# Optimization experiments

Measured on AMD Instinct MI355X. Metric: run time of the kernel, lower is better.

## Reference

```python
import jax, jax.numpy as jnp
import numpy as np

DIM = 1024
NUM_HEADS = 16
HEAD_DIM = DIM // NUM_HEADS
INNER_ITR = 4
INNER_LR = 1.0
SCALE_QKV = 1.0


def setup_inputs() -> dict:
    key = jax.random.key(0)
    k1, k2, k3 = jax.random.split(key, 3)
    B, N, C = 8, 1024, DIM
    x = jax.random.normal(k1, (B, N, C), dtype=jnp.float32)
    # Xavier-uniform-ish scaled dense kernels
    w_qkv = jax.random.normal(k2, (C, 3 * C), dtype=jnp.float32) * (1.0 / np.sqrt(C))
    w_proj = jax.random.normal(k3, (C, C), dtype=jnp.float32) * (1.0 / np.sqrt(C))
    b_proj = jnp.zeros((C,), dtype=jnp.float32)
    return {"x": x, "w_qkv": w_qkv, "w_proj": w_proj, "b_proj": b_proj, "training": 0}


def _mttt_base(q, k, v):
    """MTTT 'base' inner loop: per (B,H) linear model W,b trained by
    INNER_ITR full-batch GD steps on MSE reconstruction of v from k,
    then applied to q. Shapes: q,k,v are (B, H, N, d)."""
    B, H, N, d = q.shape
    W = jnp.zeros((B, H, d, d), dtype=q.dtype)
    b = jnp.zeros((B, H, 1, d), dtype=q.dtype)
    invN = 1.0 / N
    for _ in range(INNER_ITR):  # small fixed iteration count
        pred = jnp.einsum('bhnd,bhde->bhne', k, W) + b   # (B,H,N,d)
        err = pred - v
        gW = jnp.einsum('bhnd,bhne->bhde', k, err) * invN
        gb = jnp.mean(err, axis=2, keepdims=True)
        W = W - INNER_LR * gW
        b = b - INNER_LR * gb
    return jnp.einsum('bhnd,bhde->bhne', q, W) + b       # (B,H,N,d)


def reference(x, w_qkv, w_proj, b_proj, training):
    B, N, C = x.shape
    H, d = NUM_HEADS, HEAD_DIM
    qkv = jnp.einsum('bnc,ce->bne', x, w_qkv)            # (B,N,3C), qkv_bias=False
    qkv = qkv.reshape(B, N, 3, H, d).transpose(2, 0, 3, 1, 4)  # (3,B,H,N,d)
    qkv = qkv * SCALE_QKV
    q, k, v = qkv[0], qkv[1], qkv[2]
    # qk_norm=False -> identity; scale_q=False -> no q scaling
    out = _mttt_base(q, k, v)                            # (B,H,N,d)
    out = out.transpose(0, 2, 1, 3).reshape(B, N, C)
    out = jnp.einsum('bnc,cd->bnd', out, w_proj) + b_proj
    # proj dropout deterministic (training=False)
    return out
```

## Files before the change

kernel.cpp:

```cpp
#include <hip/hip_runtime.h>


#define SEQ    1024
#define NBATCH 8
#define DIMC   1024
#define NHEAD  16
#define HDIM   64
#define MROWS  8192
#define NQKV   3072

typedef __attribute__((ext_vector_type(8))) __bf16 bf16x8;
typedef __attribute__((ext_vector_type(4))) float  f32x4;

__device__ __forceinline__ unsigned short f2b(float f) {
  union { float f; unsigned int u; } v; v.f = f;
  unsigned int r = (v.u + 0x7FFFu + ((v.u >> 16) & 1u)) >> 16;
  return (unsigned short)r;
}
__device__ __forceinline__ float b2f(unsigned short u) {
  union { unsigned int u; float f; } v; v.u = ((unsigned int)u) << 16;
  return v.f;
}

__device__ __forceinline__ void load_lds16(const void* g, void* l) {
  __builtin_amdgcn_global_load_lds(
      (__attribute__((address_space(1))) void*)(void*)(g),
      (__attribute__((address_space(3))) void*)(l), 16, 0, 0);
}

#define FENCE asm volatile("" ::: "memory")
#define BAR   __builtin_amdgcn_s_barrier()

__global__ __launch_bounds__(256) void cvt_bf16(const float* __restrict__ in,
                                                unsigned short* __restrict__ out,
                                                int n4) {
  int i = blockIdx.x * 256 + threadIdx.x;
  if (i >= n4) return;
  float4 v = ((const float4*)in)[i];
  ushort4 o;
  o.x = f2b(v.x); o.y = f2b(v.y); o.z = f2b(v.z); o.w = f2b(v.w);
  ((ushort4*)out)[i] = o;
}

__global__ __launch_bounds__(256) void transpose_cvt(const float* __restrict__ in,
                                                     unsigned short* __restrict__ out,
                                                     int R, int Cc) {
  __shared__ unsigned short tile[32][33];
  int c0 = blockIdx.x * 32, r0 = blockIdx.y * 32;
  int tx = threadIdx.x, ty = threadIdx.y;
  for (int i = ty; i < 32; i += 8)
    tile[i][tx] = f2b(in[(size_t)(r0 + i) * Cc + c0 + tx]);
  __syncthreads();
  for (int i = ty; i < 32; i += 8)
    out[(size_t)(c0 + i) * R + r0 + tx] = tile[tx][i];
}

template <int BM, int BN, int WM, int WN, int STORE_F32>
__global__ __launch_bounds__(WM * WN * 64, 4)
void gemm_r3(const unsigned short* __restrict__ A,
             const unsigned short* __restrict__ BT,
             void* __restrict__ Cout,
             const float* __restrict__ bias,
             int N, int NBN) {
  constexpr int THREADS = WM * WN * 64;
  constexpr int TR      = THREADS / 4;
  constexpr int ABYTES  = BM * 64;
  constexpr int TBYTES  = (BM + BN) * 64;
  constexpr int CALLS   = TBYTES / (THREADS * 16);
  constexpr int NT      = 32;

  extern __shared__ __align__(16) char ldsb[];

  const int tid  = threadIdx.x;
  const int lane = tid & 63, wave = tid >> 6;
  const int wr = wave / WN, wc = wave % WN;
  const int frow = lane & 15, g4 = lane >> 4;
  const int cz = (g4 ^ (frow & 3)) * 16;

  const int cpx = gridDim.x >> 3;
  const int wg  = (blockIdx.x & 7) * cpx + (blockIdx.x >> 3);
  const int bm = wg / NBN, bn = wg % NBN;
  const size_t m0 = (size_t)bm * BM, n0 = (size_t)bn * BN;

  const int trow = tid >> 2;
  const int scol = ((tid & 3) ^ (trow & 3)) * 8;
  const unsigned short* psrc[CALLS];
#pragma unroll
  for (int c = 0; c < CALLS; ++c) {
    const int rr = c * TR + trow;
    psrc[c] = (rr < BM) ? (A + (m0 + rr) * 1024 + scol)
                        : (BT + (n0 + rr - BM) * 1024 + scol);
  }

  f32x4 acc[4][4];
  if (STORE_F32) {
#pragma unroll
    for (int j = 0; j < 4; ++j) {
      float4 bv = *(const float4*)&bias[n0 + wc * 64 + j * 16 + g4 * 4];
      f32x4 t; t[0] = bv.x; t[1] = bv.y; t[2] = bv.z; t[3] = bv.w;
#pragma unroll
      for (int i = 0; i < 4; ++i) acc[i][j] = t;
    }
  } else {
#pragma unroll
    for (int i = 0; i < 4; ++i)
#pragma unroll
      for (int j = 0; j < 4; ++j) acc[i][j] = f32x4{0.f, 0.f, 0.f, 0.f};
  }

  auto stage = [&](int tk, int buf) {
    char* base = ldsb + buf * TBYTES + wave * 1024;
#pragma unroll
    for (int c = 0; c < CALLS; ++c)
      load_lds16(psrc[c] + tk * 32, base + c * (THREADS * 16));
  };

  const int aoff = (wr * 64 + frow) * 64 + cz;
  const int boff = ABYTES + (wc * 64 + frow) * 64 + cz;

  stage(0, 0); stage(1, 1);
  asm volatile("s_waitcnt vmcnt(%0)" :: "i"(CALLS) : "memory");
  FENCE; BAR;

  int bcur = 0, bpre = 2;
#pragma unroll 1
  for (int t = 0; t < NT; ++t) {
    if (t + 2 < NT) stage(t + 2, bpre);
    const char* rb = ldsb + bcur * TBYTES;
    bf16x8 af[4], bq[4];
#pragma unroll
    for (int i = 0; i < 4; ++i) af[i] = *(const bf16x8*)(rb + aoff + i * 1024);
#pragma unroll
    for (int j = 0; j < 4; ++j) bq[j] = *(const bf16x8*)(rb + boff + j * 1024);
#pragma unroll
    for (int i = 0; i < 4; ++i)
#pragma unroll
      for (int j = 0; j < 4; ++j)
        acc[i][j] = __builtin_amdgcn_mfma_f32_16x16x32_bf16(bq[j], af[i],
                                                            acc[i][j], 0, 0, 0);
    if (t + 2 < NT) asm volatile("s_waitcnt vmcnt(%0)" :: "i"(CALLS) : "memory");
    else            asm volatile("s_waitcnt vmcnt(0)" ::: "memory");
    FENCE; BAR;
    bcur = (bcur == 2) ? 0 : bcur + 1;
    bpre = (bpre == 2) ? 0 : bpre + 1;
  }

  const size_t mbase = m0 + wr * 64 + frow;
  const size_t nbase = n0 + wc * 64 + g4 * 4;
  if (STORE_F32) {
    float* C = (float*)Cout;
#pragma unroll
    for (int i = 0; i < 4; ++i)
#pragma unroll
      for (int j = 0; j < 4; ++j) {
        float4 o; o.x = acc[i][j][0]; o.y = acc[i][j][1];
        o.z = acc[i][j][2]; o.w = acc[i][j][3];
        *(float4*)&C[(mbase + i * 16) * N + nbase + j * 16] = o;
      }
  } else {
    unsigned short* C = (unsigned short*)Cout;
#pragma unroll
    for (int i = 0; i < 4; ++i)
#pragma unroll
      for (int j = 0; j < 4; ++j) {
        ushort4 o; o.x = f2b(acc[i][j][0]); o.y = f2b(acc[i][j][1]);
        o.z = f2b(acc[i][j][2]); o.w = f2b(acc[i][j][3]);
        *(ushort4*)&C[(mbase + i * 16) * N + nbase + j * 16] = o;
      }
  }
}

__global__ __launch_bounds__(256) void transpose_kv(const unsigned short* __restrict__ qkvb,
                                                    unsigned short* __restrict__ kt,
                                                    unsigned short* __restrict__ vt) {
  __shared__ unsigned short tile[64][80];
  const int nc = blockIdx.x * 64;
  const int bh = blockIdx.y;
  const int which = blockIdx.z;
  const int b = bh >> 4, h = bh & 15;
  const int tid = threadIdx.x;
  const unsigned short* src = qkvb + (size_t)(b * SEQ + nc) * NQKV + (which + 1) * DIMC + h * HDIM;
  for (int idx = tid; idx < 512; idx += 256) {
    int rr = idx >> 3, ss = (idx & 7) * 8;
    *(uint4*)&tile[rr][ss] = *(const uint4*)&src[(size_t)rr * NQKV + ss];
  }
  __syncthreads();
  unsigned short* dst = (which ? vt : kt) + (size_t)bh * HDIM * SEQ;
  for (int idx = tid; idx < 512; idx += 256) {
    int dd = idx >> 3, ns = (idx & 7) * 8;
    alignas(16) unsigned short tmp[8];
#pragma unroll
    for (int jj = 0; jj < 8; ++jj) tmp[jj] = tile[ns + jj][dd];
    *(uint4*)&dst[(size_t)dd * SEQ + nc + ns] = *(const uint4*)tmp;
  }
}

__global__ __launch_bounds__(256) void stats_gd(const unsigned short* __restrict__ kt,
                                                const unsigned short* __restrict__ vt,
                                                unsigned short* __restrict__ Wtb,
                                                float* __restrict__ bvec) {
  __shared__ float Gs[64][68];
  __shared__ float Ps[64][68];
  __shared__ float Ws[64][68];
  __shared__ float mkp[4][64], mvp[4][64];
  __shared__ float mks[64], mvs[64], bs[64];

  const int bh = blockIdx.x;
  const int tid = threadIdx.x;
  const int lane = tid & 63, wave = tid >> 6;
  const unsigned short* kb = kt + (size_t)bh * HDIM * SEQ;
  const unsigned short* vb = vt + (size_t)bh * HDIM * SEQ;
  const int frow = lane & 15;
  const int fk = (lane >> 4) * 8;

  f32x4 accG[4], accP[4];
#pragma unroll
  for (int j = 0; j < 4; ++j) {
    accG[j] = f32x4{0.f, 0.f, 0.f, 0.f};
    accP[j] = f32x4{0.f, 0.f, 0.f, 0.f};
  }
  for (int nb = 0; nb < SEQ; nb += 32) {
    bf16x8 af = *(const bf16x8*)&kb[(size_t)(wave * 16 + frow) * SEQ + nb + fk];
    bf16x8 kf[4], vf[4];
#pragma unroll
    for (int j = 0; j < 4; ++j)
      kf[j] = *(const bf16x8*)&kb[(size_t)(j * 16 + frow) * SEQ + nb + fk];
#pragma unroll
    for (int j = 0; j < 4; ++j)
      vf[j] = *(const bf16x8*)&vb[(size_t)(j * 16 + frow) * SEQ + nb + fk];
#pragma unroll
    for (int j = 0; j < 4; ++j) {
      accG[j] = __builtin_amdgcn_mfma_f32_16x16x32_bf16(af, kf[j], accG[j], 0, 0, 0);
      accP[j] = __builtin_amdgcn_mfma_f32_16x16x32_bf16(af, vf[j], accP[j], 0, 0, 0);
    }
  }
  const float invN = 1.0f / (float)SEQ;
  const int orow = wave * 16 + (lane >> 4) * 4;
#pragma unroll
  for (int j = 0; j < 4; ++j)
#pragma unroll
    for (int r = 0; r < 4; ++r) {
      Gs[orow + r][j * 16 + frow] = accG[j][r] * invN;
      Ps[orow + r][j * 16 + frow] = accP[j][r] * invN;
    }

  {
    float sk_ = 0.f, sv_ = 0.f;
    const unsigned short* kr = &kb[(size_t)lane * SEQ + wave * 256];
    const unsigned short* vr = &vb[(size_t)lane * SEQ + wave * 256];
    for (int nn = 0; nn < 256; nn += 8) {
      uint4 a = *(const uint4*)&kr[nn];
      uint4 c = *(const uint4*)&vr[nn];
      const unsigned short* pa = (const unsigned short*)&a;
      const unsigned short* pc = (const unsigned short*)&c;
#pragma unroll
      for (int jj = 0; jj < 8; ++jj) { sk_ += b2f(pa[jj]); sv_ += b2f(pc[jj]); }
    }
    mkp[wave][lane] = sk_;
    mvp[wave][lane] = sv_;
  }
  __syncthreads();

  const int r = tid >> 2;
  const int c0 = (tid & 3) * 16;
  if (tid < 64) {
    mks[tid] = (mkp[0][tid] + mkp[1][tid] + mkp[2][tid] + mkp[3][tid]) * invN;
    mvs[tid] = (mvp[0][tid] + mvp[1][tid] + mvp[2][tid] + mvp[3][tid]) * invN;
    bs[tid] = 0.f;
  }
#pragma unroll
  for (int c = 0; c < 16; ++c) Ws[r][c0 + c] = 0.f;
  __syncthreads();

  for (int it = 0; it < 4; ++it) {
    float wn[16];
#pragma unroll
    for (int c = 0; c < 16; ++c)
      wn[c] = Ws[r][c0 + c] + Ps[r][c0 + c] - mks[r] * bs[c0 + c];
    for (int j = 0; j < 64; ++j) {
      float g = Gs[r][j];
#pragma unroll
      for (int c = 0; c < 16; ++c) wn[c] -= g * Ws[j][c0 + c];
    }
    float bn = 0.f;
    if (tid < 64) {
      bn = mvs[tid];
      for (int j = 0; j < 64; ++j) bn -= mks[j] * Ws[j][tid];
    }
    __syncthreads();
#pragma unroll
    for (int c = 0; c < 16; ++c) Ws[r][c0 + c] = wn[c];
    if (tid < 64) bs[tid] = bn;
    __syncthreads();
  }

  unsigned short* wout = Wtb + (size_t)bh * HDIM * HDIM;
#pragma unroll
  for (int c = 0; c < 16; ++c)
    wout[(size_t)(c0 + c) * HDIM + r] = f2b(Ws[r][c0 + c]);
  if (tid < 64) bvec[(size_t)bh * HDIM + tid] = bs[tid];
}

__global__ __launch_bounds__(256) void attn_qw(const unsigned short* __restrict__ qkvb,
                                               const unsigned short* __restrict__ Wtb,
                                               const float* __restrict__ bvec,
                                               unsigned short* __restrict__ attnb) {
  const int h = blockIdx.y;
  const int m0 = blockIdx.x * 128;
  const int bh = ((m0 >> 10) << 4) + h;
  const int tid = threadIdx.x;
  const int lane = tid & 63, wave = tid >> 6;
  const int frow = lane & 15;
  const int fk = (lane >> 4) * 8;

  f32x4 acc[2][4];
#pragma unroll
  for (int j = 0; j < 4; ++j) {
    float bv = bvec[(size_t)bh * HDIM + j * 16 + frow];
    f32x4 t; t[0] = bv; t[1] = bv; t[2] = bv; t[3] = bv;
    acc[0][j] = t; acc[1][j] = t;
  }

  const unsigned short* qbase = qkvb + (size_t)(m0 + wave * 32) * NQKV + h * HDIM;
  const unsigned short* wbase = Wtb + (size_t)bh * HDIM * HDIM;
#pragma unroll
  for (int s = 0; s < 2; ++s) {
    bf16x8 af[2], wf[4];
#pragma unroll
    for (int i = 0; i < 2; ++i)
      af[i] = *(const bf16x8*)&qbase[(size_t)(i * 16 + frow) * NQKV + s * 32 + fk];
#pragma unroll
    for (int j = 0; j < 4; ++j)
      wf[j] = *(const bf16x8*)&wbase[(size_t)(j * 16 + frow) * HDIM + s * 32 + fk];
#pragma unroll
    for (int i = 0; i < 2; ++i)
#pragma unroll
      for (int j = 0; j < 4; ++j)
        acc[i][j] = __builtin_amdgcn_mfma_f32_16x16x32_bf16(af[i], wf[j], acc[i][j], 0, 0, 0);
  }

  const int orow = m0 + wave * 32 + (lane >> 4) * 4;
#pragma unroll
  for (int i = 0; i < 2; ++i)
#pragma unroll
    for (int j = 0; j < 4; ++j)
#pragma unroll
      for (int rr = 0; rr < 4; ++rr)
        attnb[(size_t)(orow + i * 16 + rr) * DIMC + h * HDIM + j * 16 + frow] = f2b(acc[i][j][rr]);
}

extern "C" void kernel_launch(void* const* d_in, const int* in_sizes, int n_in,
                              void* d_out, int out_size, void* d_ws, size_t ws_size,
                              hipStream_t stream) {
  const float* x      = (const float*)d_in[0];
  const float* w_qkv  = (const float*)d_in[1];
  const float* w_proj = (const float*)d_in[2];
  const float* b_proj = (const float*)d_in[3];

  char* ws = (char*)d_ws;
  unsigned short* xb    = (unsigned short*)(ws + 0);
  unsigned short* wqT   = (unsigned short*)(ws + 16777216);
  unsigned short* wpT   = (unsigned short*)(ws + 23068672);
  unsigned short* qkvb  = (unsigned short*)(ws + 25165824);
  unsigned short* kt    = (unsigned short*)(ws + 75497472);
  unsigned short* vt    = (unsigned short*)(ws + 92274688);
  unsigned short* attnb = (unsigned short*)(ws + 109051904);
  unsigned short* Wtb   = (unsigned short*)(ws + 125829120);
  float*          bvec  = (float*)(ws + 126877696);
  if (ws_size < (size_t)126910464) return;

  hipFuncSetAttribute((const void*)gemm_r3<128, 256, 2, 4, 0>,
                      hipFuncAttributeMaxDynamicSharedMemorySize, 73728);
  hipFuncSetAttribute((const void*)gemm_r3<128, 128, 2, 2, 1>,
                      hipFuncAttributeMaxDynamicSharedMemorySize, 49152);

  cvt_bf16<<<8192, 256, 0, stream>>>(x, xb, MROWS * DIMC / 4);
  transpose_cvt<<<dim3(96, 32), dim3(32, 8), 0, stream>>>(w_qkv, wqT, 1024, 3072);
  transpose_cvt<<<dim3(32, 32), dim3(32, 8), 0, stream>>>(w_proj, wpT, 1024, 1024);
  gemm_r3<128, 256, 2, 4, 0><<<dim3(768), dim3(512), 73728, stream>>>(xb, wqT, qkvb, nullptr, NQKV, 12);
  transpose_kv<<<dim3(16, 128, 2), 256, 0, stream>>>(qkvb, kt, vt);
  stats_gd<<<128, 256, 0, stream>>>(kt, vt, Wtb, bvec);
  attn_qw<<<dim3(64, 16), 256, 0, stream>>>(qkvb, Wtb, bvec, attnb);
  gemm_r3<128, 128, 2, 2, 1><<<dim3(512), dim3(256), 49152, stream>>>(attnb, wpT, d_out, b_proj, DIMC, 8);
}
```

Before: 198.2 us.

## Fold per-head inner weights into output projection, removing attn_qw pass

The per-(batch,head) learned W and bias are folded algebraically into the output projection. A per-batch combined weight WcT = W_h·Wproj and a combined bias are built, and the final GEMM reads q directly from the qkv buffer with stride 3072 and a per-batch B matrix. This removes the attn_qw kernel and the round trip through the attn buffer. In exchange it adds the wc_build and bc_build kernels, makes the output GEMM stream a separate 1024x1024 weight per batch (more B-side traffic), and rounds the combined weight to bf16. The LDS swizzle pattern is also changed.

```diff
diff --git a/kernel.cpp b/kernel.cpp
--- a/kernel.cpp
+++ b/kernel.cpp
@@ -55,8 +55,8 @@
     out[(size_t)(c0 + i) * R + r0 + tx] = tile[tx][i];
 }
 
-template <int BM, int BN, int WM, int WN, int STORE_F32>
-__global__ __launch_bounds__(WM * WN * 64, 4)
+template <int BM, int BN, int WM, int WN, int ASTRIDE, int BMODE, int PERB>
+__device__ __forceinline__
 void gemm_r3(const unsigned short* __restrict__ A,
              const unsigned short* __restrict__ BT,
              void* __restrict__ Cout,
@@ -75,28 +75,31 @@
   const int lane = tid & 63, wave = tid >> 6;
   const int wr = wave / WN, wc = wave % WN;
   const int frow = lane & 15, g4 = lane >> 4;
-  const int cz = (g4 ^ (frow & 3)) * 16;
+  const int cz = (g4 ^ ((frow >> 1) & 3)) * 16;
 
   const int cpx = gridDim.x >> 3;
   const int wg  = (blockIdx.x & 7) * cpx + (blockIdx.x >> 3);
   const int bm = wg / NBN, bn = wg % NBN;
   const size_t m0 = (size_t)bm * BM, n0 = (size_t)bn * BN;
 
+  const unsigned short* BTb = PERB ? (BT + (m0 >> 10) * (size_t)(1024 * 1024)) : BT;
+
   const int trow = tid >> 2;
-  const int scol = ((tid & 3) ^ (trow & 3)) * 8;
+  const int scol = ((tid & 3) ^ ((tid >> 3) & 3)) * 8;
   const unsigned short* psrc[CALLS];
 #pragma unroll
   for (int c = 0; c < CALLS; ++c) {
     const int rr = c * TR + trow;
-    psrc[c] = (rr < BM) ? (A + (m0 + rr) * 1024 + scol)
-                        : (BT + (n0 + rr - BM) * 1024 + scol);
+    psrc[c] = (rr < BM) ? (A + (m0 + rr) * (size_t)ASTRIDE + scol)
+                        : (BTb + (size_t)(n0 + rr - BM) * 1024 + scol);
   }
 
   f32x4 acc[4][4];
-  if (STORE_F32) {
+  if (BMODE == 2) {
+    const float* bp = bias + (m0 >> 10) * (size_t)N;
 #pragma unroll
     for (int j = 0; j < 4; ++j) {
-      float4 bv = *(const float4*)&bias[n0 + wc * 64 + j * 16 + g4 * 4];
+      float4 bv = *(const float4*)&bp[n0 + wc * 64 + j * 16 + g4 * 4];
       f32x4 t; t[0] = bv.x; t[1] = bv.y; t[2] = bv.z; t[3] = bv.w;
 #pragma unroll
       for (int i = 0; i < 4; ++i) acc[i][j] = t;
@@ -147,7 +150,7 @@
 
   const size_t mbase = m0 + wr * 64 + frow;
   const size_t nbase = n0 + wc * 64 + g4 * 4;
-  if (STORE_F32) {
+  if (BMODE == 2) {
     float* C = (float*)Cout;
 #pragma unroll
     for (int i = 0; i < 4; ++i)
@@ -168,6 +171,19 @@
         *(ushort4*)&C[(mbase + i * 16) * N + nbase + j * 16] = o;
       }
   }
+}
+
+__global__ __launch_bounds__(512, 4) void g_qkv(const unsigned short* __restrict__ A,
+                                                const unsigned short* __restrict__ BT,
+                                                void* __restrict__ C,
+                                                const float* __restrict__ bias, int N, int NBN) {
+  gemm_r3<128, 256, 2, 4, 1024, 0, 0>(A, BT, C, bias, N, NBN);
+}
+__global__ __launch_bounds__(256, 4) void g_out(const unsigned short* __restrict__ A,
+                                                const unsigned short* __restrict__ BT,
+                                                void* __restrict__ C,
+                                                const float* __restrict__ bias, int N, int NBN) {
+  gemm_r3<128, 128, 2, 2, NQKV, 2, 1>(A, BT, C, bias, N, NBN);
 }
 
 __global__ __launch_bounds__(256) void transpose_kv(const unsigned short* __restrict__ qkvb,
@@ -197,7 +213,7 @@
 
 __global__ __launch_bounds__(256) void stats_gd(const unsigned short* __restrict__ kt,
                                                 const unsigned short* __restrict__ vt,
-                                                unsigned short* __restrict__ Wtb,
+                                                unsigned short* __restrict__ Wfb,
                                                 float* __restrict__ bvec) {
   __shared__ float Gs[64][68];
   __shared__ float Ps[64][68];
@@ -294,59 +310,74 @@
     __syncthreads();
   }
 
-  unsigned short* wout = Wtb + (size_t)bh * HDIM * HDIM;
+  unsigned short* wout = Wfb + (size_t)bh * HDIM * HDIM;
 #pragma unroll
   for (int c = 0; c < 16; ++c)
-    wout[(size_t)(c0 + c) * HDIM + r] = f2b(Ws[r][c0 + c]);
+    wout[(size_t)r * HDIM + c0 + c] = f2b(Ws[r][c0 + c]);
   if (tid < 64) bvec[(size_t)bh * HDIM + tid] = bs[tid];
 }
 
-__global__ __launch_bounds__(256) void attn_qw(const unsigned short* __restrict__ qkvb,
-                                               const unsigned short* __restrict__ Wtb,
-                                               const float* __restrict__ bvec,
-                                               unsigned short* __restrict__ attnb) {
-  const int h = blockIdx.y;
-  const int m0 = blockIdx.x * 128;
-  const int bh = ((m0 >> 10) << 4) + h;
+__global__ __launch_bounds__(256) void wc_build(const unsigned short* __restrict__ wpT,
+                                                const unsigned short* __restrict__ Wfb,
+                                                unsigned short* __restrict__ WcT) {
+  const int bh = blockIdx.x;
+  const int pblk = blockIdx.y;
+  const int b = bh >> 4, h = bh & 15;
   const int tid = threadIdx.x;
   const int lane = tid & 63, wave = tid >> 6;
-  const int frow = lane & 15;
-  const int fk = (lane >> 4) * 8;
-
-  f32x4 acc[2][4];
-#pragma unroll
-  for (int j = 0; j < 4; ++j) {
-    float bv = bvec[(size_t)bh * HDIM + j * 16 + frow];
-    f32x4 t; t[0] = bv; t[1] = bv; t[2] = bv; t[3] = bv;
-    acc[0][j] = t; acc[1][j] = t;
-  }
-
-  const unsigned short* qbase = qkvb + (size_t)(m0 + wave * 32) * NQKV + h * HDIM;
-  const unsigned short* wbase = Wtb + (size_t)bh * HDIM * HDIM;
-#pragma unroll
-  for (int s = 0; s < 2; ++s) {
-    bf16x8 af[2], wf[4];
-#pragma unroll
-    for (int i = 0; i < 2; ++i)
-      af[i] = *(const bf16x8*)&qbase[(size_t)(i * 16 + frow) * NQKV + s * 32 + fk];
+  const int frow = lane & 15, g4 = lane >> 4, fk = g4 * 8;
+  const int p0 = pblk * 256 + wave * 64;
+
+  f32x4 acc[4][4];
+#pragma unroll
+  for (int i = 0; i < 4; ++i)
+#pragma unroll
+    for (int j = 0; j < 4; ++j) acc[i][j] = f32x4{0.f, 0.f, 0.f, 0.f};
+
+  const unsigned short* wb = Wfb + (size_t)bh * 4096;
+#pragma unroll
+  for (int kk = 0; kk < 2; ++kk) {
+    bf16x8 af[4], bq[4];
+#pragma unroll
+    for (int i = 0; i < 4; ++i)
+      af[i] = *(const bf16x8*)&wpT[(size_t)(p0 + i * 16 + frow) * 1024 + h * 64 + kk * 32 + fk];
 #pragma unroll
     for (int j = 0; j < 4; ++j)
-      wf[j] = *(const bf16x8*)&wbase[(size_t)(j * 16 + frow) * HDIM + s * 32 + fk];
-#pragma unroll
-    for (int i = 0; i < 2; ++i)
+      bq[j] = *(const bf16x8*)&wb[(size_t)(j * 16 + frow) * 64 + kk * 32 + fk];
+#pragma unroll
+    for (int i = 0; i < 4; ++i)
 #pragma unroll
       for (int j = 0; j < 4; ++j)
-        acc[i][j] = __builtin_amdgcn_mfma_f32_16x16x32_bf16(af[i], wf[j], acc[i][j], 0, 0, 0);
-  }
-
-  const int orow = m0 + wave * 32 + (lane >> 4) * 4;
-#pragma unroll
-  for (int i = 0; i < 2; ++i)
-#pragma unroll
-    for (int j = 0; j < 4; ++j)
-#pragma unroll
-      for (int rr = 0; rr < 4; ++rr)
-        attnb[(size_t)(orow + i * 16 + rr) * DIMC + h * HDIM + j * 16 + frow] = f2b(acc[i][j][rr]);
+        acc[i][j] = __builtin_amdgcn_mfma_f32_16x16x32_bf16(bq[j], af[i], acc[i][j], 0, 0, 0);
+  }
+
+  unsigned short* dst = WcT + (size_t)b * 1024 * 1024;
+#pragma unroll
+  for (int i = 0; i < 4; ++i)
+#pragma unroll
+    for (int j = 0; j < 4; ++j) {
+      ushort4 o; o.x = f2b(acc[i][j][0]); o.y = f2b(acc[i][j][1]);
+      o.z = f2b(acc[i][j][2]); o.w = f2b(acc[i][j][3]);
+      *(ushort4*)&dst[(size_t)(p0 + i * 16 + frow) * 1024 + h * 64 + j * 16 + g4 * 4] = o;
+    }
+}
+
+__global__ __launch_bounds__(256) void bc_build(const float* __restrict__ wp,
+                                                const float* __restrict__ bvec,
+                                                const float* __restrict__ b_proj,
+                                                float* __restrict__ bc) {
+  const int p = blockIdx.x * 256 + threadIdx.x;
+  float s[8];
+  float bp = b_proj[p];
+#pragma unroll
+  for (int b = 0; b < 8; ++b) s[b] = bp;
+  for (int c = 0; c < 1024; ++c) {
+    float w = wp[(size_t)c * 1024 + p];
+#pragma unroll
+    for (int b = 0; b < 8; ++b) s[b] += bvec[b * 1024 + c] * w;
+  }
+#pragma unroll
+  for (int b = 0; b < 8; ++b) bc[b * 1024 + p] = s[b];
 }
 
 extern "C" void kernel_launch(void* const* d_in, const int* in_sizes, int n_in,
@@ -364,22 +395,22 @@
   unsigned short* qkvb  = (unsigned short*)(ws + 25165824);
   unsigned short* kt    = (unsigned short*)(ws + 75497472);
   unsigned short* vt    = (unsigned short*)(ws + 92274688);
-  unsigned short* attnb = (unsigned short*)(ws + 109051904);
-  unsigned short* Wtb   = (unsigned short*)(ws + 125829120);
+  unsigned short* WcT   = (unsigned short*)(ws + 109051904);
+  unsigned short* Wfb   = (unsigned short*)(ws + 125829120);
   float*          bvec  = (float*)(ws + 126877696);
-  if (ws_size < (size_t)126910464) return;
-
-  hipFuncSetAttribute((const void*)gemm_r3<128, 256, 2, 4, 0>,
-                      hipFuncAttributeMaxDynamicSharedMemorySize, 73728);
-  hipFuncSetAttribute((const void*)gemm_r3<128, 128, 2, 2, 1>,
-                      hipFuncAttributeMaxDynamicSharedMemorySize, 49152);
+  float*          bc    = (float*)(ws + 126910464);
+  if (ws_size < (size_t)126943232) return;
+
+  hipFuncSetAttribute((const void*)g_qkv, hipFuncAttributeMaxDynamicSharedMemorySize, 73728);
+  hipFuncSetAttribute((const void*)g_out, hipFuncAttributeMaxDynamicSharedMemorySize, 49152);
 
   cvt_bf16<<<8192, 256, 0, stream>>>(x, xb, MROWS * DIMC / 4);
   transpose_cvt<<<dim3(96, 32), dim3(32, 8), 0, stream>>>(w_qkv, wqT, 1024, 3072);
   transpose_cvt<<<dim3(32, 32), dim3(32, 8), 0, stream>>>(w_proj, wpT, 1024, 1024);
-  gemm_r3<128, 256, 2, 4, 0><<<dim3(768), dim3(512), 73728, stream>>>(xb, wqT, qkvb, nullptr, NQKV, 12);
+  g_qkv<<<dim3(768), dim3(512), 73728, stream>>>(xb, wqT, qkvb, nullptr, NQKV, 12);
   transpose_kv<<<dim3(16, 128, 2), 256, 0, stream>>>(qkvb, kt, vt);
-  stats_gd<<<128, 256, 0, stream>>>(kt, vt, Wtb, bvec);
-  attn_qw<<<dim3(64, 16), 256, 0, stream>>>(qkvb, Wtb, bvec, attnb);
-  gemm_r3<128, 128, 2, 2, 1><<<dim3(512), dim3(256), 49152, stream>>>(attnb, wpT, d_out, b_proj, DIMC, 8);
-}
+  stats_gd<<<128, 256, 0, stream>>>(kt, vt, Wfb, bvec);
+  wc_build<<<dim3(128, 4), 256, 0, stream>>>(wpT, Wfb, WcT);
+  bc_build<<<4, 256, 0, stream>>>(w_proj, bvec, b_proj, bc);
+  g_out<<<dim3(512), 256, 49152, stream>>>(qkvb, WcT, d_out, bc, DIMC, 8);
+}
```

Result: slower. 302.5 us (+52.6%).
